# Kernel optimization log

Measured on AMD Instinct MI355X. Metric: run time of the kernel, lower is better.

## Reference

```python
import jax, jax.numpy as jnp
import numpy as np

OLD_W, OLD_H = 224, 224   # raster image spatial size (originalShape[2:])
NEW_W, NEW_H = 28, 28     # feature-grid spatial size (newShape[2:])
B, N_SV, HID = 64, 63, 512  # batch, surrounding agents (N-1), LSTM encoder hidden
POS_SCALE = 250.0         # some positions exceed OLD_W to exercise validity masks


def setup_inputs() -> dict:
    key = jax.random.key(0)
    k1, k2, k3 = jax.random.split(key, 3)
    svPositionsAtT0 = jax.random.uniform(k1, (B, N_SV, 3), dtype=jnp.float32) * POS_SCALE
    svEncoding = jax.random.normal(k2, (B, N_SV, HID), dtype=jnp.float32)
    lengths = jax.random.randint(k3, (B,), 0, N_SV, dtype=jnp.int32)
    return {"svPositionsAtT0": svPositionsAtT0, "svEncoding": svEncoding, "lengths": lengths}


def reference(svPositionsAtT0, svEncoding, lengths):
    # Faithful vectorized form of rawToRasterScaleSocialState:
    # sequential per-agent max-writes into a zero-initialized grid == scatter-max.
    b_, n_, hid = svEncoding.shape
    x = svPositionsAtT0[..., 0]                     # (B, N)
    y = svPositionsAtT0[..., 1]
    xIdx = (x * NEW_W / OLD_W).astype(jnp.int32)    # trunc toward zero, as .long()
    yIdx = (y * NEW_H / OLD_H).astype(jnp.int32)
    agent_ids = jnp.arange(n_, dtype=lengths.dtype)[None, :]
    mask = (lengths[:, None] > agent_ids) & (xIdx < NEW_W) & (yIdx < NEW_H)  # (B, N)
    # Invalid agents: write 0 (no-op since grid init is 0 and writes are max-with-0)
    enc = jnp.where(mask[..., None], svEncoding, 0.0)          # (B, N, HID)
    xI = jnp.clip(xIdx, 0, NEW_W - 1)
    yI = jnp.clip(yIdx, 0, NEW_H - 1)
    bI = jnp.broadcast_to(jnp.arange(b_)[:, None], (b_, n_))
    grid = jnp.zeros((b_, hid, NEW_W, NEW_H), dtype=svEncoding.dtype)
    grid = grid.at[bI.ravel(), :, xI.ravel(), yI.ravel()].max(enc.reshape(b_ * n_, hid))
    return grid
```

## Files before the change

### kernel.cpp

```cpp
#include <hip/hip_runtime.h>
#include <hip/hip_bf16.h>

#define NSV    63
#define HID    512
#define GW     28
#define GH     28
#define CELLS  (GW * GH)
#define HCHUNK 16
#define NTHREADS 256
#define NF4    (HCHUNK * CELLS / 4)
#define F4ROW  (CELLS / 4)

__global__ __launch_bounds__(NTHREADS)
void scatter_grid_kernel(const float* __restrict__ pos,
                         const float* __restrict__ enc,
                         const int*   __restrict__ lengths,
                         float*       __restrict__ out) {
    const int b      = blockIdx.y;
    const int h_base = blockIdx.x * HCHUNK;
    const int t      = threadIdx.x;

    __shared__ unsigned long long mask_s[CELLS];
    __shared__ float enc_s[NSV * HCHUNK];

    for (int c = t; c < CELLS; c += NTHREADS) mask_s[c] = 0ull;

    {
        const int n = t >> 2;
        const int q = t & 3;
        if (n < NSV) {
            const float4 v = ((const float4*)(enc + ((size_t)b * NSV + n) * HID + h_base))[q];
            ((float4*)(enc_s + n * HCHUNK))[q] = v;
        }
    }
    __syncthreads();

    if (t < NSV) {
        const float x = pos[((size_t)b * NSV + t) * 3 + 0];
        const float y = pos[((size_t)b * NSV + t) * 3 + 1];
        const int len = lengths[b];
        const int xi = (int)(x * 28.0f / 224.0f);
        const int yi = (int)(y * 28.0f / 224.0f);
        if ((t < len) && (xi < GW) && (yi < GH)) {
            const int xc = min(max(xi, 0), GW - 1);
            const int yc = min(max(yi, 0), GH - 1);
            atomicOr(&mask_s[xc * GH + yc], 1ull << t);
        }
    }
    __syncthreads();

    float4* d4 = (float4*)(out + ((size_t)b * HID + h_base) * CELLS);
    for (int i = t; i < NF4; i += NTHREADS) {
        const int h = i / F4ROW;
        const int c = (i - h * F4ROW) * 4;
        float4 v = make_float4(0.f, 0.f, 0.f, 0.f);
        #pragma unroll
        for (int j = 0; j < 4; ++j) {
            unsigned long long m = mask_s[c + j];
            float val = 0.f;
            while (m) {
                const int n = __ffsll(m) - 1;
                m &= m - 1;
                val = fmaxf(val, enc_s[n * HCHUNK + h]);
            }
            (&v.x)[j] = val;
        }
        d4[i] = v;
    }
}

extern "C" void kernel_launch(void* const* d_in, const int* in_sizes, int n_in,
                              void* d_out, int out_size, void* d_ws, size_t ws_size,
                              hipStream_t stream) {
    const float* pos     = (const float*)d_in[0];
    const float* enc     = (const float*)d_in[1];
    const int*   lengths = (const int*)d_in[2];
    float*       out     = (float*)d_out;

    const int B = in_sizes[2];

    dim3 grid(HID / HCHUNK, B);
    dim3 block(NTHREADS);
    scatter_grid_kernel<<<grid, block, 0, stream>>>(pos, enc, lengths, out);
}
```

Measured before the change: 119.4 us.

## Reuse cell masks across hidden channels and vectorize shared-memory encoding reads

Each of 196 threads now owns a quad of grid cells. It loads the four 64-bit occupancy masks once and loops over all 16 hidden channels, reading float4 slices of the encoding per set bit instead of one scalar per channel. The mask array is XOR-swizzled and the encoding rows are padded to reduce LDS bank conflicts. In exchange only 196 of 256 threads do output work, and each thread issues 16 strided stores instead of the previous fully coalesced grid-stride loop.

```diff
diff --git a/kernel.cpp b/kernel.cpp
--- a/kernel.cpp
+++ b/kernel.cpp
@@ -1,5 +1,4 @@
 #include <hip/hip_runtime.h>
-#include <hip/hip_bf16.h>
 
 #define NSV    63
 #define HID    512
@@ -8,8 +7,10 @@
 #define CELLS  (GW * GH)
 #define HCHUNK 16
 #define NTHREADS 256
-#define NF4    (HCHUNK * CELLS / 4)
-#define F4ROW  (CELLS / 4)
+#define NQUADS (CELLS / 4)
+#define EPAD   20
+
+__device__ __forceinline__ int swz(int u) { return u ^ (((u >> 4) & 3) << 2); }
 
 __global__ __launch_bounds__(NTHREADS)
 void scatter_grid_kernel(const float* __restrict__ pos,
@@ -21,7 +22,7 @@
     const int t      = threadIdx.x;
 
     __shared__ unsigned long long mask_s[CELLS];
-    __shared__ float enc_s[NSV * HCHUNK];
+    __shared__ float enc_s[NSV * EPAD + 4];
 
     for (int c = t; c < CELLS; c += NTHREADS) mask_s[c] = 0ull;
 
@@ -30,7 +31,7 @@
         const int q = t & 3;
         if (n < NSV) {
             const float4 v = ((const float4*)(enc + ((size_t)b * NSV + n) * HID + h_base))[q];
-            ((float4*)(enc_s + n * HCHUNK))[q] = v;
+            *(float4*)(enc_s + n * EPAD + q * 4) = v;
         }
     }
     __syncthreads();
@@ -44,28 +45,44 @@
         if ((t < len) && (xi < GW) && (yi < GH)) {
             const int xc = min(max(xi, 0), GW - 1);
             const int yc = min(max(yi, 0), GH - 1);
-            atomicOr(&mask_s[xc * GH + yc], 1ull << t);
+            atomicOr(&mask_s[swz(xc * GH + yc)], 1ull << t);
         }
     }
     __syncthreads();
 
-    float4* d4 = (float4*)(out + ((size_t)b * HID + h_base) * CELLS);
-    for (int i = t; i < NF4; i += NTHREADS) {
-        const int h = i / F4ROW;
-        const int c = (i - h * F4ROW) * 4;
-        float4 v = make_float4(0.f, 0.f, 0.f, 0.f);
+    if (t < NQUADS) {
+        unsigned long long m0, m1, m2, m3;
+        {
+            const int base = swz(4 * t);
+            const ulonglong2 a = *(const ulonglong2*)(mask_s + base);
+            const ulonglong2 c = *(const ulonglong2*)(mask_s + base + 2);
+            m0 = a.x; m1 = a.y; m2 = c.x; m3 = c.y;
+        }
+
+        float4* d4 = (float4*)(out + ((size_t)b * HID + h_base) * CELLS);
+
         #pragma unroll
-        for (int j = 0; j < 4; ++j) {
-            unsigned long long m = mask_s[c + j];
-            float val = 0.f;
-            while (m) {
-                const int n = __ffsll(m) - 1;
-                m &= m - 1;
-                val = fmaxf(val, enc_s[n * HCHUNK + h]);
+        for (int hq = 0; hq < 4; ++hq) {
+            float4 v0 = make_float4(0.f, 0.f, 0.f, 0.f);
+            float4 v1 = v0, v2 = v0, v3 = v0;
+            #pragma unroll
+            for (int j = 0; j < 4; ++j) {
+                unsigned long long mm = (j == 0) ? m0 : (j == 1) ? m1 : (j == 2) ? m2 : m3;
+                while (mm) {
+                    const int n = __ffsll(mm) - 1;
+                    mm &= mm - 1;
+                    const float4 e = *(const float4*)(enc_s + n * EPAD + hq * 4);
+                    (&v0.x)[j] = fmaxf((&v0.x)[j], e.x);
+                    (&v1.x)[j] = fmaxf((&v1.x)[j], e.y);
+                    (&v2.x)[j] = fmaxf((&v2.x)[j], e.z);
+                    (&v3.x)[j] = fmaxf((&v3.x)[j], e.w);
+                }
             }
-            (&v.x)[j] = val;
+            d4[(hq * 4 + 0) * NQUADS + t] = v0;
+            d4[(hq * 4 + 1) * NQUADS + t] = v1;
+            d4[(hq * 4 + 2) * NQUADS + t] = v2;
+            d4[(hq * 4 + 3) * NQUADS + t] = v3;
         }
-        d4[i] = v;
     }
 }
 
```

Result: faster. 115.4 us (median of 2 runs) (-3.4%).
